# Performance work log

Hardware: AMD Instinct MI355X
Metric: run time of the kernel (lower is better)

Reference implementation:

```python
import jax, jax.numpy as jnp
import numpy as np

N_NODES = 100000
N_EDGES = 1600000
IN_FEATS = 128
OUT_FEATS = 256
K = 32


def setup_inputs() -> dict:
    key = jax.random.key(0)
    ks = jax.random.split(key, 8)
    feat = jax.random.normal(ks[0], (N_NODES, IN_FEATS), dtype=jnp.float32)
    # MaxK sparsified activations: nonnegative values (post-ReLU top-k)
    topk_values = jax.random.uniform(ks[1], (N_NODES, K), dtype=jnp.float32)
    topk_indices = jax.random.randint(ks[2], (N_NODES, K), 0, IN_FEATS, dtype=jnp.int32)
    # CSR expanded to COO: sorted row ids emulate indptr ordering
    row = jnp.sort(jax.random.randint(ks[3], (N_EDGES,), 0, N_NODES, dtype=jnp.int32))
    col = jax.random.randint(ks[4], (N_EDGES,), 0, N_NODES, dtype=jnp.int32)
    # in-degrees clamped to min 1.0, as in set_graph_data
    deg = jax.ops.segment_sum(jnp.ones((N_EDGES,), jnp.float32), row, num_segments=N_NODES)
    degrees = jnp.maximum(deg, 1.0)
    gain = float(np.sqrt(2.0))  # calculate_gain('relu')
    bnd_n = gain * np.sqrt(6.0 / (IN_FEATS + OUT_FEATS))
    W_neigh = jax.random.uniform(ks[5], (IN_FEATS, OUT_FEATS), jnp.float32, -bnd_n, bnd_n)
    W_self = jax.random.uniform(ks[6], (IN_FEATS, OUT_FEATS), jnp.float32, -bnd_n, bnd_n)
    bnd_b = 1.0 / np.sqrt(IN_FEATS)
    b_self = jax.random.uniform(ks[7], (OUT_FEATS,), jnp.float32, -bnd_b, bnd_b)
    return {"feat": feat, "topk_values": topk_values, "topk_indices": topk_indices,
            "row": row, "col": col, "degrees": degrees,
            "W_neigh": W_neigh, "W_self": W_self, "b_self": b_self}


def reference(feat, topk_values, topk_indices, row, col, degrees, W_neigh, W_self, b_self):
    n = feat.shape[0]
    # Scatter top-k sparse features back to dense [N, in_feats]
    # (real top-k indices are unique per row, so add == set; add is deterministic)
    rows = jnp.arange(n, dtype=jnp.int32)[:, None]
    x_sparse = jnp.zeros((n, IN_FEATS), feat.dtype).at[rows, topk_indices].add(topk_values)
    # CSR SpMM with all-ones edge values + degree normalization (mean aggregation)
    gathered = x_sparse[col]                                  # [E, in_feats]
    agg = jax.ops.segment_sum(gathered, row, num_segments=n)  # [N, in_feats]
    agg = agg / degrees[:, None]
    # lin_before_mp is False (in_feats <= out_feats): linear after aggregation
    h_neigh = agg @ W_neigh                                    # [N, out_feats]
    rst = feat @ W_self + b_self + h_neigh
    return rst
```

## Files before the change

kernel.cpp:

```cpp
#include <hip/hip_runtime.h>
#include <hip/hip_bf16.h>
#include <stdint.h>

#define IN_FEATS 128
#define OUT_FEATS 256
#define TOPK 32
#define BM 128
#define BN 128
#define BK 32
#define AL 40
#define KTOT 256

typedef float f32x4 __attribute__((ext_vector_type(4)));
typedef short bf16x8 __attribute__((ext_vector_type(8)));

__device__ __forceinline__ unsigned short f2bf(float x) {
    unsigned u = __float_as_uint(x);
    u += 0x7FFFu + ((u >> 16) & 1u);
    return (unsigned short)(u >> 16);
}

__global__ void k_scatter(const float* __restrict__ vals, const int* __restrict__ idxs,
                          unsigned short* __restrict__ xsp, int n_nodes) {
    __shared__ float lds[2 * IN_FEATS];
    int t = threadIdx.x;
    int n0 = blockIdx.x * 2;
    lds[t] = 0.f;
    __syncthreads();
    if (t < 2 * TOPK) {
        int h = t >> 5;
        int k = t & 31;
        int n = n0 + h;
        if (n < n_nodes) {
            float v = vals[(size_t)n * TOPK + k];
            int ix = idxs[(size_t)n * TOPK + k];
            atomicAdd(&lds[h * IN_FEATS + ix], v);
        }
    }
    __syncthreads();
    int h2 = t >> 7;
    int f = t & 127;
    int n = n0 + h2;
    if (n < n_nodes) xsp[(size_t)n * IN_FEATS + f] = f2bf(lds[t]);
}

__global__ void k_weights(const float* __restrict__ Wn, const float* __restrict__ Ws,
                          unsigned short* __restrict__ WT) {
    int idx = blockIdx.x * 256 + threadIdx.x;
    int n = idx >> 8;
    int k = idx & 255;
    float v = (k < IN_FEATS) ? Wn[(size_t)k * OUT_FEATS + n]
                             : Ws[(size_t)(k - IN_FEATS) * OUT_FEATS + n];
    WT[idx] = f2bf(v);
}

__global__ void k_indptr(const int* __restrict__ row, int* __restrict__ indptr,
                         int n_nodes, int n_edges) {
    int e = blockIdx.x * 256 + threadIdx.x;
    if (e >= n_edges) return;
    int r = row[e];
    int rp = (e == 0) ? -1 : row[e - 1];
    for (int x = rp + 1; x <= r; ++x) indptr[x] = e;
    if (e == n_edges - 1)
        for (int x = r + 1; x <= n_nodes; ++x) indptr[x] = n_edges;
}

__global__ __launch_bounds__(256) void k_aggregate(
    const unsigned short* __restrict__ xsp,
    const int* __restrict__ indptr, const int* __restrict__ col,
    unsigned short* __restrict__ agg, int n_nodes) {
    int t = threadIdx.x;
    int node = blockIdx.x * 4 + (t >> 6);
    if (node >= n_nodes) return;
    int lane = t & 63;
    int eg = lane >> 4, fi = lane & 15;
    int e0 = indptr[node], e1 = indptr[node + 1];

    float acc[8] = {0.f, 0.f, 0.f, 0.f, 0.f, 0.f, 0.f, 0.f};
    int elast = (e1 > e0) ? (e1 - 1) : e0;
    for (int base = e0; base < e1; base += 8) {
        int ea = base + eg;
        int eb = base + 4 + eg;
        float sa = (ea < e1) ? 1.f : 0.f;
        float sb = (eb < e1) ? 1.f : 0.f;
        int ca = col[ea < elast ? ea : elast];
        int cb = col[eb < elast ? eb : elast];
        uint4 ua = *(const uint4*)(xsp + (size_t)ca * IN_FEATS + fi * 8);
        uint4 ub = *(const uint4*)(xsp + (size_t)cb * IN_FEATS + fi * 8);
        unsigned pa[4] = {ua.x, ua.y, ua.z, ua.w};
        unsigned pb[4] = {ub.x, ub.y, ub.z, ub.w};
#pragma unroll
        for (int i = 0; i < 4; ++i) {
            acc[2 * i]     = fmaf(sa, __uint_as_float(pa[i] << 16), acc[2 * i]);
            acc[2 * i + 1] = fmaf(sa, __uint_as_float(pa[i] & 0xFFFF0000u), acc[2 * i + 1]);
            acc[2 * i]     = fmaf(sb, __uint_as_float(pb[i] << 16), acc[2 * i]);
            acc[2 * i + 1] = fmaf(sb, __uint_as_float(pb[i] & 0xFFFF0000u), acc[2 * i + 1]);
        }
    }
#pragma unroll
    for (int i = 0; i < 8; ++i) {
        acc[i] += __shfl_down(acc[i], 16, 64);
        acc[i] += __shfl_down(acc[i], 32, 64);
    }
    if (eg == 0) {
        int cnt = e1 - e0;
        float inv = 1.0f / (float)(cnt > 0 ? cnt : 1);
        unsigned o[4];
#pragma unroll
        for (int i = 0; i < 4; ++i) {
            unsigned lo = f2bf(acc[2 * i] * inv);
            unsigned hi = f2bf(acc[2 * i + 1] * inv);
            o[i] = lo | (hi << 16);
        }
        *(uint4*)(agg + (size_t)node * IN_FEATS + fi * 8) = *(uint4*)&o[0];
    }
}

__global__ __launch_bounds__(256) void k_gemm(
    const unsigned short* __restrict__ agg,
    const float* __restrict__ feat,
    const unsigned short* __restrict__ WT,
    const float* __restrict__ bias,
    float* __restrict__ out, int n_nodes) {
    __shared__ __align__(16) unsigned short Ash[BM * AL];
    __shared__ __align__(16) unsigned short Bsh[BN * AL];
    int t = threadIdx.x;
    int m0 = blockIdx.x * BM;
    int n0 = blockIdx.y * BN;
    int lane = t & 63;
    int w = t >> 6;
    int wr = w >> 1, wc = w & 1;
    int lrow = lane & 15, quad = lane >> 4;

    f32x4 acc[4][4];
    for (int i = 0; i < 4; ++i)
        for (int j = 0; j < 4; ++j)
            acc[i][j] = (f32x4){0.f, 0.f, 0.f, 0.f};

    for (int kk = 0; kk < KTOT; kk += BK) {
        for (int pass = 0; pass < 2; ++pass) {
            int g = t + pass * 256;
            int rowi = g >> 2;
            int q = g & 3;
            int gk = kk + q * 8;
            int node = m0 + rowi;
            if (node >= n_nodes) node = n_nodes - 1;
            uint4 v;
            if (kk < IN_FEATS) {
                v = *(const uint4*)(agg + (size_t)node * IN_FEATS + gk);
            } else {
                const float* fp = feat + (size_t)node * IN_FEATS + (gk - IN_FEATS);
                float4 f0 = *(const float4*)fp;
                float4 f1 = *(const float4*)(fp + 4);
                v.x = (unsigned)f2bf(f0.x) | ((unsigned)f2bf(f0.y) << 16);
                v.y = (unsigned)f2bf(f0.z) | ((unsigned)f2bf(f0.w) << 16);
                v.z = (unsigned)f2bf(f1.x) | ((unsigned)f2bf(f1.y) << 16);
                v.w = (unsigned)f2bf(f1.z) | ((unsigned)f2bf(f1.w) << 16);
            }
            *(uint4*)&Ash[rowi * AL + q * 8] = v;

            uint4 bv = *(const uint4*)(WT + (size_t)(n0 + rowi) * KTOT + gk);
            *(uint4*)&Bsh[rowi * AL + q * 8] = bv;
        }
        __syncthreads();

        bf16x8 af[4], bfr[4];
        for (int mi = 0; mi < 4; ++mi)
            af[mi] = *(const bf16x8*)&Ash[(wr * 64 + mi * 16 + lrow) * AL + quad * 8];
        for (int ni = 0; ni < 4; ++ni)
            bfr[ni] = *(const bf16x8*)&Bsh[(wc * 64 + ni * 16 + lrow) * AL + quad * 8];
        for (int mi = 0; mi < 4; ++mi)
            for (int ni = 0; ni < 4; ++ni)
                acc[mi][ni] = __builtin_amdgcn_mfma_f32_16x16x32_bf16(
                    af[mi], bfr[ni], acc[mi][ni], 0, 0, 0);
        __syncthreads();
    }

    for (int mi = 0; mi < 4; ++mi) {
        int gm = m0 + wr * 64 + mi * 16 + quad * 4;
        for (int ni = 0; ni < 4; ++ni) {
            int go = n0 + wc * 64 + ni * 16 + lrow;
            float b = bias[go];
            for (int r = 0; r < 4; ++r) {
                int node = gm + r;
                if (node < n_nodes)
                    out[(size_t)node * OUT_FEATS + go] = acc[mi][ni][r] + b;
            }
        }
    }
}

extern "C" void kernel_launch(void* const* d_in, const int* in_sizes, int n_in,
                              void* d_out, int out_size, void* d_ws, size_t ws_size,
                              hipStream_t stream) {
    const float* feat = (const float*)d_in[0];
    const float* tkv  = (const float*)d_in[1];
    const int*   tki  = (const int*)d_in[2];
    const int*   row  = (const int*)d_in[3];
    const int*   col  = (const int*)d_in[4];
    const float* Wn   = (const float*)d_in[6];
    const float* Ws   = (const float*)d_in[7];
    const float* bias = (const float*)d_in[8];
    float* out = (float*)d_out;

    int n_nodes = in_sizes[5];
    int n_edges = in_sizes[3];

    unsigned short* xsp = (unsigned short*)d_ws;
    unsigned short* agg = xsp + (size_t)n_nodes * IN_FEATS;
    unsigned short* WT  = agg + (size_t)n_nodes * IN_FEATS;
    int* indptr = (int*)(WT + (size_t)OUT_FEATS * KTOT);

    k_scatter<<<(n_nodes + 1) / 2, 256, 0, stream>>>(tkv, tki, xsp, n_nodes);
    k_weights<<<256, 256, 0, stream>>>(Wn, Ws, WT);
    k_indptr<<<(n_edges + 255) / 256, 256, 0, stream>>>(row, indptr, n_nodes, n_edges);
    k_aggregate<<<(n_nodes + 3) / 4, 256, 0, stream>>>(xsp, indptr, col, agg, n_nodes);
    dim3 g3((n_nodes + BM - 1) / BM, OUT_FEATS / BN);
    k_gemm<<<g3, 256, 0, stream>>>(agg, feat, WT, bias, out, n_nodes);
}
```

Measured before the change: 305.4 us.

## Fuse feat bf16 conversion into aggregate and use async global-to-LDS loads in GEMM

The aggregation kernel now also converts each node's feat row to bf16 and writes it next to the aggregated features in a concatenated [N,256] bf16 matrix. The GEMM then reads a single bf16 A operand and stages both A and B tiles with global_load_lds direct-to-LDS copies in a fragment-ordered layout, with no register staging or padding. This removes the per-tile fp32-to-bf16 conversion in the GEMM, which is otherwise repeated for each of the two N-column blocks, and shortens the load path. In exchange it adds an extra bf16 feat write to the workspace, and the direct-to-LDS copies still finish before the MFMAs start, so loads and compute do not overlap.

```diff
diff --git a/kernel.cpp b/kernel.cpp
--- a/kernel.cpp
+++ b/kernel.cpp
@@ -8,7 +8,6 @@
 #define BM 128
 #define BN 128
 #define BK 32
-#define AL 40
 #define KTOT 256
 
 typedef float f32x4 __attribute__((ext_vector_type(4)));
@@ -18,6 +17,12 @@
     unsigned u = __float_as_uint(x);
     u += 0x7FFFu + ((u >> 16) & 1u);
     return (unsigned short)(u >> 16);
+}
+
+__device__ __forceinline__ void async16(const void* g, void* l) {
+    __builtin_amdgcn_global_load_lds(
+        (const __attribute__((address_space(1))) unsigned*)g,
+        (__attribute__((address_space(3))) unsigned*)l, 16, 0, 0);
 }
 
 __global__ void k_scatter(const float* __restrict__ vals, const int* __restrict__ idxs,
@@ -67,14 +72,17 @@
 
 __global__ __launch_bounds__(256) void k_aggregate(
     const unsigned short* __restrict__ xsp,
+    const float* __restrict__ feat,
     const int* __restrict__ indptr, const int* __restrict__ col,
-    unsigned short* __restrict__ agg, int n_nodes) {
+    unsigned short* __restrict__ Acat, int n_nodes) {
     int t = threadIdx.x;
     int node = blockIdx.x * 4 + (t >> 6);
     if (node >= n_nodes) return;
     int lane = t & 63;
     int eg = lane >> 4, fi = lane & 15;
     int e0 = indptr[node], e1 = indptr[node + 1];
+
+    float2 fv = *(const float2*)(feat + (size_t)node * IN_FEATS + lane * 2);
 
     float acc[8] = {0.f, 0.f, 0.f, 0.f, 0.f, 0.f, 0.f, 0.f};
     int elast = (e1 > e0) ? (e1 - 1) : e0;
@@ -97,6 +105,9 @@
             acc[2 * i + 1] = fmaf(sb, __uint_as_float(pb[i] & 0xFFFF0000u), acc[2 * i + 1]);
         }
     }
+    unsigned pk = (unsigned)f2bf(fv.x) | ((unsigned)f2bf(fv.y) << 16);
+    *(unsigned*)(Acat + (size_t)node * KTOT + IN_FEATS + lane * 2) = pk;
+
 #pragma unroll
     for (int i = 0; i < 8; ++i) {
         acc[i] += __shfl_down(acc[i], 16, 64);
@@ -112,18 +123,17 @@
             unsigned hi = f2bf(acc[2 * i + 1] * inv);
             o[i] = lo | (hi << 16);
         }
-        *(uint4*)(agg + (size_t)node * IN_FEATS + fi * 8) = *(uint4*)&o[0];
+        *(uint4*)(Acat + (size_t)node * KTOT + fi * 8) = *(uint4*)&o[0];
     }
 }
 
 __global__ __launch_bounds__(256) void k_gemm(
-    const unsigned short* __restrict__ agg,
-    const float* __restrict__ feat,
+    const unsigned short* __restrict__ Acat,
     const unsigned short* __restrict__ WT,
     const float* __restrict__ bias,
     float* __restrict__ out, int n_nodes) {
-    __shared__ __align__(16) unsigned short Ash[BM * AL];
-    __shared__ __align__(16) unsigned short Bsh[BN * AL];
+    __shared__ __align__(16) unsigned short Ash[BM * BK];
+    __shared__ __align__(16) unsigned short Bsh[BN * BK];
     int t = threadIdx.x;
     int m0 = blockIdx.x * BM;
     int n0 = blockIdx.y * BN;
@@ -131,6 +141,7 @@
     int w = t >> 6;
     int wr = w >> 1, wc = w & 1;
     int lrow = lane & 15, quad = lane >> 4;
+    int g = lane >> 4, r = lane & 15;
 
     f32x4 acc[4][4];
     for (int i = 0; i < 4; ++i)
@@ -138,38 +149,27 @@
             acc[i][j] = (f32x4){0.f, 0.f, 0.f, 0.f};
 
     for (int kk = 0; kk < KTOT; kk += BK) {
-        for (int pass = 0; pass < 2; ++pass) {
-            int g = t + pass * 256;
-            int rowi = g >> 2;
-            int q = g & 3;
-            int gk = kk + q * 8;
-            int node = m0 + rowi;
-            if (node >= n_nodes) node = n_nodes - 1;
-            uint4 v;
-            if (kk < IN_FEATS) {
-                v = *(const uint4*)(agg + (size_t)node * IN_FEATS + gk);
-            } else {
-                const float* fp = feat + (size_t)node * IN_FEATS + (gk - IN_FEATS);
-                float4 f0 = *(const float4*)fp;
-                float4 f1 = *(const float4*)(fp + 4);
-                v.x = (unsigned)f2bf(f0.x) | ((unsigned)f2bf(f0.y) << 16);
-                v.y = (unsigned)f2bf(f0.z) | ((unsigned)f2bf(f0.w) << 16);
-                v.z = (unsigned)f2bf(f1.x) | ((unsigned)f2bf(f1.y) << 16);
-                v.w = (unsigned)f2bf(f1.z) | ((unsigned)f2bf(f1.w) << 16);
-            }
-            *(uint4*)&Ash[rowi * AL + q * 8] = v;
-
-            uint4 bv = *(const uint4*)(WT + (size_t)(n0 + rowi) * KTOT + gk);
-            *(uint4*)&Bsh[rowi * AL + q * 8] = bv;
+#pragma unroll
+        for (int p = 0; p < 2; ++p) {
+            int seg = 2 * w + p;
+            int arow = m0 + seg * 16 + r;
+            if (arow > n_nodes - 1) arow = n_nodes - 1;
+            async16(Acat + (size_t)arow * KTOT + kk + g * 8, &Ash[seg * 512]);
+            int brow = n0 + seg * 16 + r;
+            async16(WT + (size_t)brow * KTOT + kk + g * 8, &Bsh[seg * 512]);
         }
         __syncthreads();
 
         bf16x8 af[4], bfr[4];
+#pragma unroll
         for (int mi = 0; mi < 4; ++mi)
-            af[mi] = *(const bf16x8*)&Ash[(wr * 64 + mi * 16 + lrow) * AL + quad * 8];
+            af[mi] = *(const bf16x8*)&Ash[(wr * 4 + mi) * 512 + quad * 128 + lrow * 8];
+#pragma unroll
         for (int ni = 0; ni < 4; ++ni)
-            bfr[ni] = *(const bf16x8*)&Bsh[(wc * 64 + ni * 16 + lrow) * AL + quad * 8];
+            bfr[ni] = *(const bf16x8*)&Bsh[(wc * 4 + ni) * 512 + quad * 128 + lrow * 8];
+#pragma unroll
         for (int mi = 0; mi < 4; ++mi)
+#pragma unroll
             for (int ni = 0; ni < 4; ++ni)
                 acc[mi][ni] = __builtin_amdgcn_mfma_f32_16x16x32_bf16(
                     af[mi], bfr[ni], acc[mi][ni], 0, 0, 0);
@@ -181,10 +181,10 @@
         for (int ni = 0; ni < 4; ++ni) {
             int go = n0 + wc * 64 + ni * 16 + lrow;
             float b = bias[go];
-            for (int r = 0; r < 4; ++r) {
-                int node = gm + r;
+            for (int rr = 0; rr < 4; ++rr) {
+                int node = gm + rr;
                 if (node < n_nodes)
-                    out[(size_t)node * OUT_FEATS + go] = acc[mi][ni][r] + b;
+                    out[(size_t)node * OUT_FEATS + go] = acc[mi][ni][rr] + b;
             }
         }
     }
@@ -206,15 +206,15 @@
     int n_nodes = in_sizes[5];
     int n_edges = in_sizes[3];
 
-    unsigned short* xsp = (unsigned short*)d_ws;
-    unsigned short* agg = xsp + (size_t)n_nodes * IN_FEATS;
-    unsigned short* WT  = agg + (size_t)n_nodes * IN_FEATS;
+    unsigned short* xsp  = (unsigned short*)d_ws;
+    unsigned short* Acat = xsp + (size_t)n_nodes * IN_FEATS;
+    unsigned short* WT   = Acat + (size_t)n_nodes * KTOT;
     int* indptr = (int*)(WT + (size_t)OUT_FEATS * KTOT);
 
     k_scatter<<<(n_nodes + 1) / 2, 256, 0, stream>>>(tkv, tki, xsp, n_nodes);
     k_weights<<<256, 256, 0, stream>>>(Wn, Ws, WT);
     k_indptr<<<(n_edges + 255) / 256, 256, 0, stream>>>(row, indptr, n_nodes, n_edges);
-    k_aggregate<<<(n_nodes + 3) / 4, 256, 0, stream>>>(xsp, indptr, col, agg, n_nodes);
+    k_aggregate<<<(n_nodes + 3) / 4, 256, 0, stream>>>(xsp, feat, indptr, col, Acat, n_nodes);
     dim3 g3((n_nodes + BM - 1) / BM, OUT_FEATS / BN);
-    k_gemm<<<g3, 256, 0, stream>>>(agg, feat, WT, bias, out, n_nodes);
-}
+    k_gemm<<<g3, 256, 0, stream>>>(Acat, WT, bias, out, n_nodes);
+}
```

After: 314.1 us. +2.8%, slower.
